# Kernel tuning notes

Hardware: AMD Instinct MI355X
Metric: run time of the kernel (lower is better)

## Reference

```python
import jax, jax.numpy as jnp
import numpy as np

BRIGHT_THRESH = 0.65
SAT_THRESH = 0.15
SMOOTH_K = 15
LAMBDA_L1 = 1.0
LAMBDA_WIN_L1 = 3.0
LAMBDA_WIN_COLOR = 1.0
WINDOW_WEIGHT = 5.0
BASE_WEIGHT = 1.0
TRANSFORM_WEIGHT = 2.0
EPS = 1e-8


def _avg_pool_same(x, k=SMOOTH_K):
    # AvgPool2d(k, stride=1, padding=k//2), count_include_pad=True (torch default)
    p = k // 2
    s = jax.lax.reduce_window(x, 0.0, jax.lax.add, (1, 1, k, k), (1, 1, 1, 1),
                              [(0, 0), (0, 0), (p, p), (p, p)])
    return s / (k * k)


def _window_detector(source):
    # Rescale from [-1,1] to [0,1] if any negative values present
    src = jnp.where(source.min() < 0, (source + 1) * 0.5, source)
    brightness = 0.299 * src[:, 0:1] + 0.587 * src[:, 1:2] + 0.114 * src[:, 2:3]
    bright_mask = jax.nn.sigmoid(20.0 * (brightness - BRIGHT_THRESH))
    saturation = src.max(axis=1, keepdims=True) - src.min(axis=1, keepdims=True)
    low_sat_mask = jax.nn.sigmoid(20.0 * (SAT_THRESH - saturation))
    return _avg_pool_same(bright_mask * low_sat_mask)


def _normalize_ch(x):
    # F.normalize over channel dim with eps clamp
    n = jnp.sqrt(jnp.sum(x * x, axis=1, keepdims=True))
    return x / jnp.maximum(n, EPS)


def setup_inputs() -> dict:
    key = jax.random.key(0)
    k1, k2, k3 = jax.random.split(key, 3)
    shape = (16, 3, 512, 512)
    return {
        "pred": jax.random.normal(k1, shape, dtype=jnp.float32),
        "target": jax.random.normal(k2, shape, dtype=jnp.float32),
        "source": jax.random.normal(k3, shape, dtype=jnp.float32),
    }


def reference(pred, target, source):
    window_mask = _window_detector(source)  # [B,1,H,W]

    # plain L1
    l1_loss = jnp.abs(pred - target).mean()

    # window-weighted L1
    weight_map = BASE_WEIGHT + (WINDOW_WEIGHT - BASE_WEIGHT) * window_mask
    win_l1_loss = (jnp.abs(pred - target) * weight_map).mean()

    # window color-transform loss
    st = target - source  # source -> target direction
    sp = pred - source    # source -> pred direction
    alignment = jnp.sum(_normalize_ch(st) * _normalize_ch(sp), axis=1, keepdims=True)
    st_mag = jnp.sqrt(jnp.sum(st * st, axis=1, keepdims=True))
    sp_mag = jnp.sqrt(jnp.sum(sp * sp, axis=1, keepdims=True))
    mag_loss = jnp.abs(sp_mag / (st_mag + EPS) - 1.0)
    color_loss = TRANSFORM_WEIGHT * (window_mask * (1.0 - alignment + 0.5 * mag_loss)).mean()

    total = LAMBDA_L1 * l1_loss + LAMBDA_WIN_L1 * win_l1_loss + LAMBDA_WIN_COLOR * color_loss
    return total
```

## Files before the change

### kernel.cpp

```cpp
#include <hip/hip_runtime.h>
#include <math.h>

#define W 512
#define H 512
#define BATCH 16
#define HW (W * H)
#define NPIX (BATCH * HW)
#define NELEM (3 * NPIX)

#define MAIN_BLOCKS 4096

__global__ __launch_bounds__(256) void k_mask_hblur(const float* __restrict__ src,
                                                    float* __restrict__ hsum) {
    __shared__ float m[528];
    const int row = blockIdx.x;
    const int b = row >> 9;
    const int y = row & (H - 1);
    const float* s0 = src + (size_t)b * 3 * HW + (size_t)y * W;
    const int t = threadIdx.x;

    if (t < 7) { m[t] = 0.f; m[519 + t] = 0.f; }

    float2 r  = *(const float2*)(s0 + 2 * t);
    float2 g  = *(const float2*)(s0 + HW + 2 * t);
    float2 bl = *(const float2*)(s0 + 2 * HW + 2 * t);
    float rv[2] = {r.x, r.y}, gv[2] = {g.x, g.y}, bv[2] = {bl.x, bl.y};

#pragma unroll
    for (int j = 0; j < 2; ++j) {
        float R = (rv[j] + 1.f) * 0.5f;
        float G = (gv[j] + 1.f) * 0.5f;
        float B = (bv[j] + 1.f) * 0.5f;
        float bright = 0.299f * R + 0.587f * G + 0.114f * B;
        float mx = fmaxf(R, fmaxf(G, B));
        float mn = fminf(R, fminf(G, B));
        float sat = mx - mn;
        float bm = 1.f / (1.f + __expf(-20.f * (bright - 0.65f)));
        float sm = 1.f / (1.f + __expf(-20.f * (0.15f - sat)));
        m[7 + 2 * t + j] = bm * sm;
    }
    __syncthreads();

    float* orow = hsum + (size_t)row * W;
    float h[2];
#pragma unroll
    for (int j = 0; j < 2; ++j) {
        const int x = 2 * t + j;
        float acc = 0.f;
#pragma unroll
        for (int k = 0; k < 15; ++k) acc += m[x + k];
        h[j] = acc;
    }
    *(float2*)(orow + 2 * t) = make_float2(h[0], h[1]);
}

__global__ __launch_bounds__(256) void k_main(const float* __restrict__ pred,
                                              const float* __restrict__ targ,
                                              const float* __restrict__ srcp,
                                              const float* __restrict__ hsum,
                                              float* __restrict__ partials) {
    const int tid = blockIdx.x * 256 + threadIdx.x;
    const int p4 = tid * 4;
    const int b = p4 >> 18;
    const int rem = p4 & (HW - 1);
    const int y = rem >> 9;
    const int x = rem & (W - 1);

    const size_t base = (size_t)b * 3 * HW + (size_t)y * W + x;
    const float4 pR = *(const float4*)(pred + base);
    const float4 pG = *(const float4*)(pred + base + HW);
    const float4 pB = *(const float4*)(pred + base + 2 * HW);
    const float4 tR = *(const float4*)(targ + base);
    const float4 tG = *(const float4*)(targ + base + HW);
    const float4 tB = *(const float4*)(targ + base + 2 * HW);
    const float4 sR = *(const float4*)(srcp + base);
    const float4 sG = *(const float4*)(srcp + base + HW);
    const float4 sB = *(const float4*)(srcp + base + 2 * HW);

    float4 v = make_float4(0.f, 0.f, 0.f, 0.f);
    const float* hb = hsum + (size_t)b * HW + x;
#pragma unroll
    for (int dy = -7; dy <= 7; ++dy) {
        const int yy = y + dy;
        if ((unsigned)yy < (unsigned)H) {
            const float4 hv = *(const float4*)(hb + (size_t)yy * W);
            v.x += hv.x; v.y += hv.y; v.z += hv.z; v.w += hv.w;
        }
    }
    const float inv225 = 1.f / 225.f;
    const float wm[4] = {v.x * inv225, v.y * inv225, v.z * inv225, v.w * inv225};

    const float pr[4] = {pR.x, pR.y, pR.z, pR.w}, pg[4] = {pG.x, pG.y, pG.z, pG.w},
                pb[4] = {pB.x, pB.y, pB.z, pB.w};
    const float tr[4] = {tR.x, tR.y, tR.z, tR.w}, tg[4] = {tG.x, tG.y, tG.z, tG.w},
                tb[4] = {tB.x, tB.y, tB.z, tB.w};
    const float sr[4] = {sR.x, sR.y, sR.z, sR.w}, sg[4] = {sG.x, sG.y, sG.z, sG.w},
                sb[4] = {sB.x, sB.y, sB.z, sB.w};

    float sA = 0.f, sAW = 0.f, sC = 0.f;
#pragma unroll
    for (int j = 0; j < 4; ++j) {
        const float a = fabsf(pr[j] - tr[j]) + fabsf(pg[j] - tg[j]) + fabsf(pb[j] - tb[j]);
        const float stx = tr[j] - sr[j], sty = tg[j] - sg[j], stz = tb[j] - sb[j];
        const float spx = pr[j] - sr[j], spy = pg[j] - sg[j], spz = pb[j] - sb[j];
        const float dot = stx * spx + sty * spy + stz * spz;
        const float st2 = stx * stx + sty * sty + stz * stz;
        const float sp2 = spx * spx + spy * spy + spz * spz;
        const float stm = sqrtf(st2);
        const float spm = sqrtf(sp2);
        const float align = dot / (fmaxf(stm, 1e-8f) * fmaxf(spm, 1e-8f));
        const float mag = fabsf(spm / (stm + 1e-8f) - 1.f);
        const float c = 1.f - align + 0.5f * mag;
        sA  += a;
        sAW += a * wm[j];
        sC  += c * wm[j];
    }

#pragma unroll
    for (int off = 32; off > 0; off >>= 1) {
        sA  += __shfl_down(sA, off);
        sAW += __shfl_down(sAW, off);
        sC  += __shfl_down(sC, off);
    }
    __shared__ float red[3][4];
    const int lane = threadIdx.x & 63;
    const int wave = threadIdx.x >> 6;
    if (lane == 0) { red[0][wave] = sA; red[1][wave] = sAW; red[2][wave] = sC; }
    __syncthreads();
    if (threadIdx.x == 0) {
        partials[(size_t)blockIdx.x * 3 + 0] = red[0][0] + red[0][1] + red[0][2] + red[0][3];
        partials[(size_t)blockIdx.x * 3 + 1] = red[1][0] + red[1][1] + red[1][2] + red[1][3];
        partials[(size_t)blockIdx.x * 3 + 2] = red[2][0] + red[2][1] + red[2][2] + red[2][3];
    }
}

__global__ __launch_bounds__(256) void k_final(const float* __restrict__ partials,
                                               float* __restrict__ out) {
    double a = 0.0, aw = 0.0, c = 0.0;
    for (int i = threadIdx.x; i < MAIN_BLOCKS; i += 256) {
        a  += (double)partials[(size_t)i * 3 + 0];
        aw += (double)partials[(size_t)i * 3 + 1];
        c  += (double)partials[(size_t)i * 3 + 2];
    }
#pragma unroll
    for (int off = 32; off > 0; off >>= 1) {
        a  += __shfl_down(a, off);
        aw += __shfl_down(aw, off);
        c  += __shfl_down(c, off);
    }
    __shared__ double rd[3][4];
    const int lane = threadIdx.x & 63;
    const int wave = threadIdx.x >> 6;
    if (lane == 0) { rd[0][wave] = a; rd[1][wave] = aw; rd[2][wave] = c; }
    __syncthreads();
    if (threadIdx.x == 0) {
        const double A  = rd[0][0] + rd[0][1] + rd[0][2] + rd[0][3];
        const double AW = rd[1][0] + rd[1][1] + rd[1][2] + rd[1][3];
        const double C  = rd[2][0] + rd[2][1] + rd[2][2] + rd[2][3];
        const double N = (double)NELEM;
        const double M = (double)NPIX;
        out[0] = (float)((4.0 * A + 12.0 * AW) / N + 2.0 * C / M);
    }
}

extern "C" void kernel_launch(void* const* d_in, const int* in_sizes, int n_in,
                              void* d_out, int out_size, void* d_ws, size_t ws_size,
                              hipStream_t stream) {
    const float* pred = (const float*)d_in[0];
    const float* targ = (const float*)d_in[1];
    const float* src  = (const float*)d_in[2];

    float* hsum     = (float*)d_ws;
    float* partials = (float*)((char*)d_ws + (size_t)NPIX * sizeof(float));

    k_mask_hblur<<<BATCH * H, 256, 0, stream>>>(src, hsum);
    k_main<<<MAIN_BLOCKS, 256, 0, stream>>>(pred, targ, src, hsum, partials);
    k_final<<<1, 256, 0, stream>>>(partials, (float*)d_out);
}
```

Baseline: 177.0 us.

## Fuse mask computation and box blur into tiled main kernel with shared-memory halo

Replaces the separate mask/horizontal-blur kernel and the main kernel with one tiled kernel. Each 64x32 tile computes the window mask over its halo in shared memory, runs sliding-window horizontal and vertical sums there, then evaluates the loss terms. This removes the global hsum write and its fifteen-row reread, plus one launch. In exchange, source pixels in the halo are recomputed (about 1.9x tile area), and the halo loads are scalar and uncoalesced.

Result: no change. 173.8 us (-1.8%).

```diff
diff --git a/kernel.cpp b/kernel.cpp
--- a/kernel.cpp
+++ b/kernel.cpp
@@ -8,112 +8,130 @@
 #define NPIX (BATCH * HW)
 #define NELEM (3 * NPIX)
 
-#define MAIN_BLOCKS 4096
+#define TW 64
+#define TH 32
+#define TILES_X (W / TW)
+#define TILES_Y (H / TH)
+#define TILES_PER_IMG (TILES_X * TILES_Y)
+#define NBLOCKS (BATCH * TILES_PER_IMG)
 
-__global__ __launch_bounds__(256) void k_mask_hblur(const float* __restrict__ src,
-                                                    float* __restrict__ hsum) {
-    __shared__ float m[528];
-    const int row = blockIdx.x;
-    const int b = row >> 9;
-    const int y = row & (H - 1);
-    const float* s0 = src + (size_t)b * 3 * HW + (size_t)y * W;
-    const int t = threadIdx.x;
+#define MROWS (TH + 14)
+#define MCOLS (TW + 14)
+#define MSTRIDE 81
+#define HSTRIDE 68
 
-    if (t < 7) { m[t] = 0.f; m[519 + t] = 0.f; }
+__global__ __launch_bounds__(256, 4) void k_fused(const float* __restrict__ pred,
+                                                  const float* __restrict__ targ,
+                                                  const float* __restrict__ srcp,
+                                                  float* __restrict__ partials) {
+    __shared__ float smask[MROWS * MSTRIDE];
+    __shared__ __align__(16) float shsum[MROWS * HSTRIDE];
 
-    float2 r  = *(const float2*)(s0 + 2 * t);
-    float2 g  = *(const float2*)(s0 + HW + 2 * t);
-    float2 bl = *(const float2*)(s0 + 2 * HW + 2 * t);
-    float rv[2] = {r.x, r.y}, gv[2] = {g.x, g.y}, bv[2] = {bl.x, bl.y};
+    const int tid = threadIdx.x;
+    const int bid = blockIdx.x;
+    const int b  = bid >> 7;
+    const int tl = bid & 127;
+    const int ty = tl >> 3;
+    const int tx = tl & 7;
+    const int y0 = ty * TH;
+    const int x0 = tx * TW;
+    const size_t ibase = (size_t)b * 3 * HW;
 
-#pragma unroll
-    for (int j = 0; j < 2; ++j) {
-        float R = (rv[j] + 1.f) * 0.5f;
-        float G = (gv[j] + 1.f) * 0.5f;
-        float B = (bv[j] + 1.f) * 0.5f;
-        float bright = 0.299f * R + 0.587f * G + 0.114f * B;
-        float mx = fmaxf(R, fmaxf(G, B));
-        float mn = fminf(R, fminf(G, B));
-        float sat = mx - mn;
-        float bm = 1.f / (1.f + __expf(-20.f * (bright - 0.65f)));
-        float sm = 1.f / (1.f + __expf(-20.f * (0.15f - sat)));
-        m[7 + 2 * t + j] = bm * sm;
+    for (int idx = tid; idx < MROWS * MCOLS; idx += 256) {
+        const int row = idx / MCOLS;
+        const int col = idx - row * MCOLS;
+        const int gy = y0 - 7 + row;
+        const int gx = x0 - 7 + col;
+        float mval = 0.f;
+        if ((unsigned)gy < (unsigned)H && (unsigned)gx < (unsigned)W) {
+            const size_t o = ibase + (size_t)gy * W + gx;
+            const float R = (srcp[o]          + 1.f) * 0.5f;
+            const float G = (srcp[o + HW]     + 1.f) * 0.5f;
+            const float B = (srcp[o + 2 * HW] + 1.f) * 0.5f;
+            const float bright = 0.299f * R + 0.587f * G + 0.114f * B;
+            const float sat = fmaxf(R, fmaxf(G, B)) - fminf(R, fminf(G, B));
+            const float bm = 1.f / (1.f + __expf(-20.f * (bright - 0.65f)));
+            const float sm = 1.f / (1.f + __expf(-20.f * (0.15f - sat)));
+            mval = bm * sm;
+        }
+        smask[row * MSTRIDE + col] = mval;
     }
     __syncthreads();
 
-    float* orow = hsum + (size_t)row * W;
-    float h[2];
-#pragma unroll
-    for (int j = 0; j < 2; ++j) {
-        const int x = 2 * t + j;
+    if (tid < MROWS * 2) {
+        const int r = tid >> 1;
+        const int h = tid & 1;
+        const float* mr = smask + r * MSTRIDE + 32 * h;
+        float* hr = shsum + r * HSTRIDE + 32 * h;
         float acc = 0.f;
 #pragma unroll
-        for (int k = 0; k < 15; ++k) acc += m[x + k];
-        h[j] = acc;
-    }
-    *(float2*)(orow + 2 * t) = make_float2(h[0], h[1]);
-}
-
-__global__ __launch_bounds__(256) void k_main(const float* __restrict__ pred,
-                                              const float* __restrict__ targ,
-                                              const float* __restrict__ srcp,
-                                              const float* __restrict__ hsum,
-                                              float* __restrict__ partials) {
-    const int tid = blockIdx.x * 256 + threadIdx.x;
-    const int p4 = tid * 4;
-    const int b = p4 >> 18;
-    const int rem = p4 & (HW - 1);
-    const int y = rem >> 9;
-    const int x = rem & (W - 1);
-
-    const size_t base = (size_t)b * 3 * HW + (size_t)y * W + x;
-    const float4 pR = *(const float4*)(pred + base);
-    const float4 pG = *(const float4*)(pred + base + HW);
-    const float4 pB = *(const float4*)(pred + base + 2 * HW);
-    const float4 tR = *(const float4*)(targ + base);
-    const float4 tG = *(const float4*)(targ + base + HW);
-    const float4 tB = *(const float4*)(targ + base + 2 * HW);
-    const float4 sR = *(const float4*)(srcp + base);
-    const float4 sG = *(const float4*)(srcp + base + HW);
-    const float4 sB = *(const float4*)(srcp + base + 2 * HW);
-
-    float4 v = make_float4(0.f, 0.f, 0.f, 0.f);
-    const float* hb = hsum + (size_t)b * HW + x;
-#pragma unroll
-    for (int dy = -7; dy <= 7; ++dy) {
-        const int yy = y + dy;
-        if ((unsigned)yy < (unsigned)H) {
-            const float4 hv = *(const float4*)(hb + (size_t)yy * W);
-            v.x += hv.x; v.y += hv.y; v.z += hv.z; v.w += hv.w;
+        for (int k = 0; k < 15; ++k) acc += mr[k];
+        for (int i = 0; i < 32; ++i) {
+            hr[i] = acc;
+            if (i < 31) acc += mr[i + 15] - mr[i];
         }
     }
-    const float inv225 = 1.f / 225.f;
-    const float wm[4] = {v.x * inv225, v.y * inv225, v.z * inv225, v.w * inv225};
+    __syncthreads();
 
-    const float pr[4] = {pR.x, pR.y, pR.z, pR.w}, pg[4] = {pG.x, pG.y, pG.z, pG.w},
-                pb[4] = {pB.x, pB.y, pB.z, pB.w};
-    const float tr[4] = {tR.x, tR.y, tR.z, tR.w}, tg[4] = {tG.x, tG.y, tG.z, tG.w},
-                tb[4] = {tB.x, tB.y, tB.z, tB.w};
-    const float sr[4] = {sR.x, sR.y, sR.z, sR.w}, sg[4] = {sG.x, sG.y, sG.z, sG.w},
-                sb[4] = {sB.x, sB.y, sB.z, sB.w};
+    const int cg = tid & 15;
+    const int rg = tid >> 4;
+    const int ro0 = 2 * rg;
+    const int gx = x0 + 4 * cg;
+
+    float4 S = make_float4(0.f, 0.f, 0.f, 0.f);
+#pragma unroll
+    for (int k = 0; k < 15; ++k) {
+        const float4 hv = *(const float4*)(shsum + (ro0 + k) * HSTRIDE + 4 * cg);
+        S.x += hv.x; S.y += hv.y; S.z += hv.z; S.w += hv.w;
+    }
 
     float sA = 0.f, sAW = 0.f, sC = 0.f;
+    const float inv225 = 1.f / 225.f;
+
 #pragma unroll
-    for (int j = 0; j < 4; ++j) {
-        const float a = fabsf(pr[j] - tr[j]) + fabsf(pg[j] - tg[j]) + fabsf(pb[j] - tb[j]);
-        const float stx = tr[j] - sr[j], sty = tg[j] - sg[j], stz = tb[j] - sb[j];
-        const float spx = pr[j] - sr[j], spy = pg[j] - sg[j], spz = pb[j] - sb[j];
-        const float dot = stx * spx + sty * spy + stz * spz;
-        const float st2 = stx * stx + sty * sty + stz * stz;
-        const float sp2 = spx * spx + spy * spy + spz * spz;
-        const float stm = sqrtf(st2);
-        const float spm = sqrtf(sp2);
-        const float align = dot / (fmaxf(stm, 1e-8f) * fmaxf(spm, 1e-8f));
-        const float mag = fabsf(spm / (stm + 1e-8f) - 1.f);
-        const float c = 1.f - align + 0.5f * mag;
-        sA  += a;
-        sAW += a * wm[j];
-        sC  += c * wm[j];
+    for (int i = 0; i < 2; ++i) {
+        const int ro = ro0 + i;
+        if (i == 1) {
+            const float4 hadd = *(const float4*)(shsum + (ro0 + 15) * HSTRIDE + 4 * cg);
+            const float4 hsub = *(const float4*)(shsum + ro0 * HSTRIDE + 4 * cg);
+            S.x += hadd.x - hsub.x; S.y += hadd.y - hsub.y;
+            S.z += hadd.z - hsub.z; S.w += hadd.w - hsub.w;
+        }
+        const float wm[4] = {S.x * inv225, S.y * inv225, S.z * inv225, S.w * inv225};
+
+        const size_t base = ibase + (size_t)(y0 + ro) * W + gx;
+        const float4 pR = *(const float4*)(pred + base);
+        const float4 pG = *(const float4*)(pred + base + HW);
+        const float4 pB = *(const float4*)(pred + base + 2 * HW);
+        const float4 tR = *(const float4*)(targ + base);
+        const float4 tG = *(const float4*)(targ + base + HW);
+        const float4 tB = *(const float4*)(targ + base + 2 * HW);
+        const float4 sR = *(const float4*)(srcp + base);
+        const float4 sG = *(const float4*)(srcp + base + HW);
+        const float4 sB = *(const float4*)(srcp + base + 2 * HW);
+
+        const float pr[4] = {pR.x, pR.y, pR.z, pR.w}, pg[4] = {pG.x, pG.y, pG.z, pG.w},
+                    pb[4] = {pB.x, pB.y, pB.z, pB.w};
+        const float tr[4] = {tR.x, tR.y, tR.z, tR.w}, tg[4] = {tG.x, tG.y, tG.z, tG.w},
+                    tb[4] = {tB.x, tB.y, tB.z, tB.w};
+        const float sr[4] = {sR.x, sR.y, sR.z, sR.w}, sg[4] = {sG.x, sG.y, sG.z, sG.w},
+                    sb[4] = {sB.x, sB.y, sB.z, sB.w};
+
+#pragma unroll
+        for (int j = 0; j < 4; ++j) {
+            const float a = fabsf(pr[j] - tr[j]) + fabsf(pg[j] - tg[j]) + fabsf(pb[j] - tb[j]);
+            const float stx = tr[j] - sr[j], sty = tg[j] - sg[j], stz = tb[j] - sb[j];
+            const float spx = pr[j] - sr[j], spy = pg[j] - sg[j], spz = pb[j] - sb[j];
+            const float dot = stx * spx + sty * spy + stz * spz;
+            const float stm = sqrtf(stx * stx + sty * sty + stz * stz);
+            const float spm = sqrtf(spx * spx + spy * spy + spz * spz);
+            const float align = dot / (fmaxf(stm, 1e-8f) * fmaxf(spm, 1e-8f));
+            const float mag = fabsf(spm / (stm + 1e-8f) - 1.f);
+            const float c = 1.f - align + 0.5f * mag;
+            sA  += a;
+            sAW += a * wm[j];
+            sC  += c * wm[j];
+        }
     }
 
 #pragma unroll
@@ -123,21 +141,21 @@
         sC  += __shfl_down(sC, off);
     }
     __shared__ float red[3][4];
-    const int lane = threadIdx.x & 63;
-    const int wave = threadIdx.x >> 6;
+    const int lane = tid & 63;
+    const int wave = tid >> 6;
     if (lane == 0) { red[0][wave] = sA; red[1][wave] = sAW; red[2][wave] = sC; }
     __syncthreads();
-    if (threadIdx.x == 0) {
-        partials[(size_t)blockIdx.x * 3 + 0] = red[0][0] + red[0][1] + red[0][2] + red[0][3];
-        partials[(size_t)blockIdx.x * 3 + 1] = red[1][0] + red[1][1] + red[1][2] + red[1][3];
-        partials[(size_t)blockIdx.x * 3 + 2] = red[2][0] + red[2][1] + red[2][2] + red[2][3];
+    if (tid == 0) {
+        partials[(size_t)bid * 3 + 0] = red[0][0] + red[0][1] + red[0][2] + red[0][3];
+        partials[(size_t)bid * 3 + 1] = red[1][0] + red[1][1] + red[1][2] + red[1][3];
+        partials[(size_t)bid * 3 + 2] = red[2][0] + red[2][1] + red[2][2] + red[2][3];
     }
 }
 
 __global__ __launch_bounds__(256) void k_final(const float* __restrict__ partials,
                                                float* __restrict__ out) {
     double a = 0.0, aw = 0.0, c = 0.0;
-    for (int i = threadIdx.x; i < MAIN_BLOCKS; i += 256) {
+    for (int i = threadIdx.x; i < NBLOCKS; i += 256) {
         a  += (double)partials[(size_t)i * 3 + 0];
         aw += (double)partials[(size_t)i * 3 + 1];
         c  += (double)partials[(size_t)i * 3 + 2];
@@ -170,10 +188,8 @@
     const float* targ = (const float*)d_in[1];
     const float* src  = (const float*)d_in[2];
 
-    float* hsum     = (float*)d_ws;
-    float* partials = (float*)((char*)d_ws + (size_t)NPIX * sizeof(float));
+    float* partials = (float*)d_ws;
 
-    k_mask_hblur<<<BATCH * H, 256, 0, stream>>>(src, hsum);
-    k_main<<<MAIN_BLOCKS, 256, 0, stream>>>(pred, targ, src, hsum, partials);
+    k_fused<<<NBLOCKS, 256, 0, stream>>>(pred, targ, src, partials);
     k_final<<<1, 256, 0, stream>>>(partials, (float*)d_out);
 }
```
